# Kernel optimization log

Measured on AMD Instinct MI355X. Metric: run time of the kernel, lower is better.

The kernel has to match this reference:

```python
import jax, jax.numpy as jnp
import numpy as np

N = 50000      # nodes
E = 800000     # edges (avg degree 16)
IN = 128       # in_features
H = 4          # num_heads
OUT = 32       # out_features per head
NEG_SLOPE = 0.2


def setup_inputs() -> dict:
    key = jax.random.key(0)
    k1, k2, k3, k4 = jax.random.split(key, 4)
    h = jax.random.normal(k1, (N, IN), dtype=jnp.float32)
    edge_index = jax.random.randint(k2, (2, E), 0, N, dtype=jnp.int32)
    # xavier-ish init scales
    W = jax.random.normal(k3, (H, IN, OUT), dtype=jnp.float32) * np.float32(np.sqrt(2.0 / (IN + OUT)))
    a = jax.random.normal(k4, (H, 2 * OUT), dtype=jnp.float32) * np.float32(np.sqrt(2.0 / (2 * OUT)))
    return {"h": h, "edge_index": edge_index, "W": W, "a": a}


def reference(h, edge_index, W, a):
    src, dst = edge_index[0], edge_index[1]
    # project per head: [N, H, OUT]
    h_proj = jnp.einsum('ni,hio->nho', h, W)
    # score = leaky_relu(a . [Wh_src || Wh_dst]) ; split a to avoid materializing the concat
    a_src, a_dst = a[:, :OUT], a[:, OUT:]
    s_src = jnp.einsum('nho,ho->nh', h_proj, a_src)   # [N, H]
    s_dst = jnp.einsum('nho,ho->nh', h_proj, a_dst)   # [N, H]
    score = jax.nn.leaky_relu(s_src[src] + s_dst[dst], negative_slope=NEG_SLOPE)  # [E, H]
    # sparse softmax over incoming edges of each dst node
    smax = jax.ops.segment_max(score, dst, num_segments=N)          # [N, H]
    smax = jnp.where(jnp.isfinite(smax), smax, jnp.float32(-1e9))   # nodes with no in-edges
    score_exp = jnp.exp(score - smax[dst])                          # [E, H]
    denom = jax.ops.segment_sum(score_exp, dst, num_segments=N)     # [N, H]
    denom = jnp.maximum(denom, jnp.float32(1e-16))
    alpha = score_exp / denom[dst]                                  # [E, H]
    # weighted aggregation (dropout is identity in eval mode)
    h_src = h_proj[src]                                             # [E, H, OUT]
    h_out = jax.ops.segment_sum(alpha[:, :, None] * h_src, dst, num_segments=N)  # [N, H, OUT]
    h_out = h_out.reshape(N, H * OUT)  # concat=True
    return jax.nn.elu(h_out)
```

## Files before the change

kernel.cpp:

```cpp
#include <hip/hip_runtime.h>

#define NEG_SLOPE 0.2f
#define BCAP 8192

typedef __attribute__((ext_vector_type(8))) short short8;
typedef __attribute__((ext_vector_type(4))) float floatx4;

__device__ __forceinline__ unsigned f2bf(float x) {
  unsigned u = __float_as_uint(x);
  unsigned r = ((u >> 16) & 1u) + 0x7fffu;
  return (u + r) >> 16;
}
__device__ __forceinline__ float bf2f(unsigned hi16) {
  return __uint_as_float(hi16 << 16);
}

__global__ __launch_bounds__(256) void k_gemm(const float* __restrict__ h,
                                              const float* __restrict__ W,
                                              const float* __restrict__ a,
                                              const int* __restrict__ ei,
                                              int* __restrict__ bcur,
                                              unsigned* __restrict__ gpairs,
                                              unsigned short* __restrict__ hp16,
                                              float* __restrict__ ssrc,
                                              float* __restrict__ sdst,
                                              int N, int E, int NB1, int NB2) {
  __shared__ unsigned lds_u[16384];
  const int tid = threadIdx.x;

  if (blockIdx.x < NB1) {
    uint2* stage = (uint2*)lds_u;
    int* cnt = (int*)&lds_u[8192];
    int* start = (int*)&lds_u[8448];
    int* cur = (int*)&lds_u[8704];
    int* gbase = (int*)&lds_u[8960];
    int* scn = (int*)&lds_u[9216];
    const int e0 = blockIdx.x * 4096;
    for (int i = tid; i < NB2; i += 256) cnt[i] = 0;
    __syncthreads();
    int sarr[16], darr[16];
#pragma unroll
    for (int j = 0; j < 16; ++j) {
      int e = e0 + j * 256 + tid;
      if (e < E) {
        sarr[j] = ei[e];
        darr[j] = ei[E + e];
        atomicAdd(&cnt[darr[j] >> 8], 1);
      } else {
        darr[j] = -1;
      }
    }
    __syncthreads();
    int s = (tid < NB2) ? cnt[tid] : 0;
    scn[tid] = s;
    __syncthreads();
    for (int off = 1; off < 256; off <<= 1) {
      int t = (tid >= off) ? scn[tid - off] : 0;
      __syncthreads();
      scn[tid] += t;
      __syncthreads();
    }
    if (tid < NB2) {
      start[tid] = scn[tid] - s;
      cur[tid] = scn[tid] - s;
      gbase[tid] = s ? atomicAdd(&bcur[tid], s) : 0;
    }
    __syncthreads();
#pragma unroll
    for (int j = 0; j < 16; ++j) {
      if (darr[j] >= 0) {
        int b = darr[j] >> 8;
        int pos = atomicAdd(&cur[b], 1);
        stage[pos] = make_uint2((unsigned)sarr[j], (unsigned)darr[j]);
      }
    }
    __syncthreads();
    const int total = start[NB2 - 1] + cnt[NB2 - 1];
    for (int u = tid; u < total; u += 256) {
      uint2 pr = stage[u];
      int b = (int)(pr.y >> 8);
      gpairs[(size_t)b * BCAP + gbase[b] + (u - start[b])] =
          pr.x | ((pr.y & 255u) << 24);
    }
    __syncthreads();
  }

  const int lane = tid & 63;
  const int wv = tid >> 6;
  const int quad = lane >> 4;
  const int l16 = lane & 15;

#pragma unroll
  for (int it = 0; it < 8; ++it) {
    const int u = it * 256 + tid;
    const int ln = u & 63;
    const int kc = (u >> 6) & 3;
    const int ct = u >> 8;
    const int n = ct * 16 + (ln & 15);
    const int kb = kc * 32 + (ln >> 4) * 8;
    const int head = n >> 5;
    const float* src = W + head * 4096 + (size_t)kb * 32 + (n & 31);
    unsigned hi[4], lo[4];
#pragma unroll
    for (int jj = 0; jj < 4; ++jj) {
      float w0 = src[(2 * jj) * 32];
      float w1 = src[(2 * jj + 1) * 32];
      unsigned h0 = f2bf(w0), h1 = f2bf(w1);
      unsigned l0 = f2bf(w0 - bf2f(h0)), l1 = f2bf(w1 - bf2f(h1));
      hi[jj] = h0 | (h1 << 16);
      lo[jj] = l0 | (l1 << 16);
    }
    *(uint4*)&lds_u[u * 4] = make_uint4(hi[0], hi[1], hi[2], hi[3]);
    *(uint4*)&lds_u[8192 + u * 4] = make_uint4(lo[0], lo[1], lo[2], lo[3]);
  }

  const int row0 = blockIdx.x * 64;
  const int r = row0 + wv * 16 + l16;
  short8 Ah[4], Al[4];
#pragma unroll
  for (int kc = 0; kc < 4; ++kc) {
    float v[8];
    if (r < N) {
      float4 fa = *(const float4*)&h[(size_t)r * 128 + kc * 32 + quad * 8];
      float4 fb = *(const float4*)&h[(size_t)r * 128 + kc * 32 + quad * 8 + 4];
      v[0] = fa.x; v[1] = fa.y; v[2] = fa.z; v[3] = fa.w;
      v[4] = fb.x; v[5] = fb.y; v[6] = fb.z; v[7] = fb.w;
    } else {
#pragma unroll
      for (int j = 0; j < 8; ++j) v[j] = 0.f;
    }
#pragma unroll
    for (int j = 0; j < 8; ++j) {
      unsigned hi = f2bf(v[j]);
      Ah[kc][j] = (short)hi;
      Al[kc][j] = (short)f2bf(v[j] - bf2f(hi));
    }
  }
  __syncthreads();

  floatx4 C[8];
#pragma unroll
  for (int ct = 0; ct < 8; ++ct) {
    floatx4 c = {0.f, 0.f, 0.f, 0.f};
#pragma unroll
    for (int kc = 0; kc < 4; ++kc) {
      int bidx = ((ct * 4 + kc) * 64 + lane) * 4;
      short8 Bh, Bl;
      *(uint4*)&Bh = *(const uint4*)&lds_u[bidx];
      *(uint4*)&Bl = *(const uint4*)&lds_u[8192 + bidx];
      c = __builtin_amdgcn_mfma_f32_16x16x32_bf16(Ah[kc], Bh, c, 0, 0, 0);
      c = __builtin_amdgcn_mfma_f32_16x16x32_bf16(Al[kc], Bh, c, 0, 0, 0);
      c = __builtin_amdgcn_mfma_f32_16x16x32_bf16(Ah[kc], Bl, c, 0, 0, 0);
    }
    C[ct] = c;
  }
  __syncthreads();

  float* epi = (float*)lds_u;
#pragma unroll
  for (int ct = 0; ct < 8; ++ct) {
#pragma unroll
    for (int reg = 0; reg < 4; ++reg) {
      int rr = wv * 16 + quad * 4 + reg;
      epi[rr * 132 + ct * 16 + l16] = C[ct][reg];
    }
  }
  __syncthreads();

  const int row_l = tid >> 2;
  const int hh = tid & 3;
  const int rg = row0 + row_l;
  if (rg < N) {
    const float* rowp = &epi[row_l * 132 + hh * 32];
    float ss = 0.f, sd = 0.f;
    unsigned pka[16];
#pragma unroll
    for (int e = 0; e < 8; ++e) {
      float4 c4 = *(const float4*)&rowp[e * 4];
      float4 as = *(const float4*)&a[hh * 64 + e * 4];
      float4 ad = *(const float4*)&a[hh * 64 + 32 + e * 4];
      ss += c4.x * as.x + c4.y * as.y + c4.z * as.z + c4.w * as.w;
      sd += c4.x * ad.x + c4.y * ad.y + c4.z * ad.z + c4.w * ad.w;
      pka[e * 2] = f2bf(c4.x) | (f2bf(c4.y) << 16);
      pka[e * 2 + 1] = f2bf(c4.z) | (f2bf(c4.w) << 16);
    }
    unsigned short* dst = &hp16[(size_t)rg * 128 + hh * 32];
    *(uint4*)(dst) = make_uint4(pka[0], pka[1], pka[2], pka[3]);
    *(uint4*)(dst + 8) = make_uint4(pka[4], pka[5], pka[6], pka[7]);
    *(uint4*)(dst + 16) = make_uint4(pka[8], pka[9], pka[10], pka[11]);
    *(uint4*)(dst + 24) = make_uint4(pka[12], pka[13], pka[14], pka[15]);
    ssrc[(size_t)rg * 4 + hh] = ss;
    sdst[(size_t)rg * 4 + hh] = sd;
  }
}

__global__ __launch_bounds__(1024) void k_sortagg(const int* __restrict__ bcur,
                                                  const unsigned* __restrict__ gpairs,
                                                  const float* __restrict__ ssrc,
                                                  const float* __restrict__ sdst,
                                                  const uint4* __restrict__ hp4,
                                                  float* __restrict__ out, int N) {
  __shared__ int cnt2[128], start2[128], cur2[128], lds[128];
  __shared__ int srcsort[4096];
  __shared__ float sdl[512];
  const int tid = threadIdx.x;
  const int u0 = blockIdx.x;
  const int chunk = gridDim.x >> 3;
  const int id = ((gridDim.x & 7) == 0) ? (u0 & 7) * chunk + (u0 >> 3) : u0;
  const int b = id >> 1;
  const int half = id & 1;
  const size_t base = (size_t)b * BCAP;
  const int size = min(bcur[b], BCAP);
  const int d0s = (b << 8) + half * 128;
  const int ndst = min(128, N - d0s);

  if (tid < 128) cnt2[tid] = 0;
  for (int i = tid; i < ndst * 4; i += 1024) sdl[i] = sdst[(size_t)d0s * 4 + i];
  __syncthreads();

  unsigned pr[8];
  int rel[8];
#pragma unroll
  for (int j = 0; j < 8; ++j) {
    const int u = tid + j * 1024;
    pr[j] = (u < size) ? gpairs[base + u] : 0xffffffffu;
    rel[j] = (int)(pr[j] >> 24) - half * 128;
    if (pr[j] == 0xffffffffu || (unsigned)rel[j] >= 128u) rel[j] = -1;
  }
#pragma unroll
  for (int j = 0; j < 8; ++j)
    if (rel[j] >= 0) atomicAdd(&cnt2[rel[j]], 1);
  __syncthreads();

  if (tid < 128) lds[tid] = cnt2[tid];
  __syncthreads();
  for (int off = 1; off < 128; off <<= 1) {
    const int t = (tid < 128 && tid >= off) ? lds[tid - off] : 0;
    __syncthreads();
    if (tid < 128) lds[tid] += t;
    __syncthreads();
  }
  if (tid < 128) {
    start2[tid] = lds[tid] - cnt2[tid];
    cur2[tid] = lds[tid] - cnt2[tid];
  }
  __syncthreads();

#pragma unroll
  for (int j = 0; j < 8; ++j) {
    if (rel[j] >= 0) {
      const int pos = atomicAdd(&cur2[rel[j]], 1);
      srcsort[pos] = (int)(pr[j] & 0x00ffffffu);
    }
  }
  __syncthreads();

  const int l = tid & 15;
  const int hh = l >> 2;
  for (int dl = tid >> 4; dl < ndst; dl += 64) {
    const int d = d0s + dl;
    const int beg = start2[dl];
    const int end = beg + cnt2[dl];
    const float sdv = sdl[dl * 4 + hh];

    float den[4] = {0.f, 0.f, 0.f, 0.f};
    float acc[8];
#pragma unroll
    for (int j = 0; j < 8; ++j) acc[j] = 0.f;

    int p = beg;
    for (; p + 3 < end; p += 4) {
      int s[4];
      float w[4];
      uint4 v[4];
#pragma unroll
      for (int q = 0; q < 4; ++q) s[q] = srcsort[p + q];
#pragma unroll
      for (int q = 0; q < 4; ++q) {
        float x = ssrc[(size_t)s[q] * 4 + hh] + sdv;
        x = x >= 0.f ? x : NEG_SLOPE * x;
        w[q] = __expf(x);
        v[q] = hp4[(size_t)s[q] * 16 + l];
      }
#pragma unroll
      for (int q = 0; q < 4; ++q) {
        den[q] += w[q];
        acc[0] = fmaf(w[q], bf2f(v[q].x & 0xffffu), acc[0]);
        acc[1] = fmaf(w[q], bf2f(v[q].x >> 16), acc[1]);
        acc[2] = fmaf(w[q], bf2f(v[q].y & 0xffffu), acc[2]);
        acc[3] = fmaf(w[q], bf2f(v[q].y >> 16), acc[3]);
        acc[4] = fmaf(w[q], bf2f(v[q].z & 0xffffu), acc[4]);
        acc[5] = fmaf(w[q], bf2f(v[q].z >> 16), acc[5]);
        acc[6] = fmaf(w[q], bf2f(v[q].w & 0xffffu), acc[6]);
        acc[7] = fmaf(w[q], bf2f(v[q].w >> 16), acc[7]);
      }
    }
    for (; p < end; ++p) {
      const int s0 = srcsort[p];
      float x = ssrc[(size_t)s0 * 4 + hh] + sdv;
      x = x >= 0.f ? x : NEG_SLOPE * x;
      const float w0 = __expf(x);
      const uint4 v0 = hp4[(size_t)s0 * 16 + l];
      den[0] += w0;
      acc[0] = fmaf(w0, bf2f(v0.x & 0xffffu), acc[0]);
      acc[1] = fmaf(w0, bf2f(v0.x >> 16), acc[1]);
      acc[2] = fmaf(w0, bf2f(v0.y & 0xffffu), acc[2]);
      acc[3] = fmaf(w0, bf2f(v0.y >> 16), acc[3]);
      acc[4] = fmaf(w0, bf2f(v0.z & 0xffffu), acc[4]);
      acc[5] = fmaf(w0, bf2f(v0.z >> 16), acc[5]);
      acc[6] = fmaf(w0, bf2f(v0.w & 0xffffu), acc[6]);
      acc[7] = fmaf(w0, bf2f(v0.w >> 16), acc[7]);
    }
    const float rden = 1.f / fmaxf((den[0] + den[1]) + (den[2] + den[3]), 1e-16f);
    float o[8];
#pragma unroll
    for (int j = 0; j < 8; ++j) {
      const float x = acc[j] * rden;
      o[j] = x > 0.f ? x : expm1f(x);
    }
    float* dst = &out[(size_t)d * 128 + l * 8];
    *(float4*)dst = make_float4(o[0], o[1], o[2], o[3]);
    *(float4*)(dst + 4) = make_float4(o[4], o[5], o[6], o[7]);
  }
}

extern "C" void kernel_launch(void* const* d_in, const int* in_sizes, int n_in,
                              void* d_out, int out_size, void* d_ws, size_t ws_size,
                              hipStream_t stream) {
  const float* h = (const float*)d_in[0];
  const int* ei = (const int*)d_in[1];
  const float* W = (const float*)d_in[2];
  const float* a = (const float*)d_in[3];
  float* out = (float*)d_out;
  const int N = in_sizes[0] / 128;
  const int E = in_sizes[1] / 2;
  const int NB2 = (N + 255) >> 8;
  const int NB1 = (E + 4095) / 4096;
  const int NBG = max((N + 63) / 64, NB1);

  char* ws = (char*)d_ws;
  unsigned short* hp16 = (unsigned short*)ws;
  unsigned* gpairs = (unsigned*)(hp16 + (size_t)N * 128);
  float* ssrc = (float*)(gpairs + (size_t)NB2 * BCAP);
  float* sdst = ssrc + (size_t)N * 4;
  int* bcur = (int*)(sdst + (size_t)N * 4);

  hipMemsetAsync(bcur, 0, NB2 * sizeof(int), stream);
  k_gemm<<<NBG, 256, 0, stream>>>(h, W, a, ei, bcur, gpairs, hp16, ssrc, sdst,
                                  N, E, NB1, NB2);
  k_sortagg<<<NB2 * 2, 1024, 0, stream>>>(bcur, gpairs, ssrc, sdst,
                                          (const uint4*)hp16, out, N);
}
```

Before: 141.9 us.

## Split sort-aggregate into quarter-bucket blocks of 512 threads

Each destination bucket of 256 nodes is now handled by four 512-thread blocks of 64 destinations instead of two 1024-thread blocks of 128. The grid doubles, giving more, smaller blocks for better occupancy and load balance across CUs. The cost is that each block re-reads the whole bucket's pair list, so the gpairs reads grow from two passes per bucket to four blocks each scanning it twice. The register-held pairs become strided loops, and srcsort writes are clamped to SCAP for safety.

```diff
diff --git a/kernel.cpp b/kernel.cpp
--- a/kernel.cpp
+++ b/kernel.cpp
@@ -2,6 +2,7 @@
 
 #define NEG_SLOPE 0.2f
 #define BCAP 8192
+#define SCAP 4096
 
 typedef __attribute__((ext_vector_type(8))) short short8;
 typedef __attribute__((ext_vector_type(4))) float floatx4;
@@ -194,73 +195,69 @@
   }
 }
 
-__global__ __launch_bounds__(1024) void k_sortagg(const int* __restrict__ bcur,
-                                                  const unsigned* __restrict__ gpairs,
-                                                  const float* __restrict__ ssrc,
-                                                  const float* __restrict__ sdst,
-                                                  const uint4* __restrict__ hp4,
-                                                  float* __restrict__ out, int N) {
-  __shared__ int cnt2[128], start2[128], cur2[128], lds[128];
-  __shared__ int srcsort[4096];
-  __shared__ float sdl[512];
+__global__ __launch_bounds__(512) void k_sortagg(const int* __restrict__ bcur,
+                                                 const unsigned* __restrict__ gpairs,
+                                                 const float* __restrict__ ssrc,
+                                                 const float* __restrict__ sdst,
+                                                 const uint4* __restrict__ hp4,
+                                                 float* __restrict__ out, int N) {
+  __shared__ int cnt2[64], start2[64], cur2[64], lds[64];
+  __shared__ int srcsort[SCAP];
+  __shared__ float sdl[256];
   const int tid = threadIdx.x;
   const int u0 = blockIdx.x;
   const int chunk = gridDim.x >> 3;
   const int id = ((gridDim.x & 7) == 0) ? (u0 & 7) * chunk + (u0 >> 3) : u0;
-  const int b = id >> 1;
-  const int half = id & 1;
+  const int b = id >> 2;
+  const int quarter = id & 3;
   const size_t base = (size_t)b * BCAP;
   const int size = min(bcur[b], BCAP);
-  const int d0s = (b << 8) + half * 128;
-  const int ndst = min(128, N - d0s);
-
-  if (tid < 128) cnt2[tid] = 0;
-  for (int i = tid; i < ndst * 4; i += 1024) sdl[i] = sdst[(size_t)d0s * 4 + i];
-  __syncthreads();
-
-  unsigned pr[8];
-  int rel[8];
-#pragma unroll
-  for (int j = 0; j < 8; ++j) {
-    const int u = tid + j * 1024;
-    pr[j] = (u < size) ? gpairs[base + u] : 0xffffffffu;
-    rel[j] = (int)(pr[j] >> 24) - half * 128;
-    if (pr[j] == 0xffffffffu || (unsigned)rel[j] >= 128u) rel[j] = -1;
-  }
-#pragma unroll
-  for (int j = 0; j < 8; ++j)
-    if (rel[j] >= 0) atomicAdd(&cnt2[rel[j]], 1);
-  __syncthreads();
-
-  if (tid < 128) lds[tid] = cnt2[tid];
-  __syncthreads();
-  for (int off = 1; off < 128; off <<= 1) {
-    const int t = (tid < 128 && tid >= off) ? lds[tid - off] : 0;
-    __syncthreads();
-    if (tid < 128) lds[tid] += t;
-    __syncthreads();
-  }
-  if (tid < 128) {
+  const int q0 = quarter * 64;
+  const int d0s = (b << 8) + q0;
+  const int ndst = min(64, N - d0s);
+
+  if (tid < 64) cnt2[tid] = 0;
+  for (int i = tid; i < ndst * 4; i += 512) sdl[i] = sdst[(size_t)d0s * 4 + i];
+  __syncthreads();
+
+  for (int u = tid; u < size; u += 512) {
+    const int rel = (int)(gpairs[base + u] >> 24) - q0;
+    if ((unsigned)rel < 64u) atomicAdd(&cnt2[rel], 1);
+  }
+  __syncthreads();
+
+  if (tid < 64) lds[tid] = cnt2[tid];
+  __syncthreads();
+  for (int off = 1; off < 64; off <<= 1) {
+    const int t = (tid < 64 && tid >= off) ? lds[tid - off] : 0;
+    __syncthreads();
+    if (tid < 64) lds[tid] += t;
+    __syncthreads();
+  }
+  if (tid < 64) {
     start2[tid] = lds[tid] - cnt2[tid];
     cur2[tid] = lds[tid] - cnt2[tid];
   }
   __syncthreads();
 
-#pragma unroll
-  for (int j = 0; j < 8; ++j) {
-    if (rel[j] >= 0) {
-      const int pos = atomicAdd(&cur2[rel[j]], 1);
-      srcsort[pos] = (int)(pr[j] & 0x00ffffffu);
+  for (int u = tid; u < size; u += 512) {
+    const unsigned pr = gpairs[base + u];
+    const int rel = (int)(pr >> 24) - q0;
+    if ((unsigned)rel < 64u) {
+      const int pos = atomicAdd(&cur2[rel], 1);
+      if (pos < SCAP) srcsort[pos] = (int)(pr & 0x00ffffffu);
     }
   }
   __syncthreads();
 
   const int l = tid & 15;
   const int hh = l >> 2;
-  for (int dl = tid >> 4; dl < ndst; dl += 64) {
+  for (int dl = tid >> 4; dl < ndst; dl += 32) {
     const int d = d0s + dl;
-    const int beg = start2[dl];
-    const int end = beg + cnt2[dl];
+    int beg = start2[dl];
+    int end = beg + cnt2[dl];
+    beg = min(beg, SCAP);
+    end = min(end, SCAP);
     const float sdv = sdl[dl * 4 + hh];
 
     float den[4] = {0.f, 0.f, 0.f, 0.f};
@@ -348,6 +345,6 @@
   hipMemsetAsync(bcur, 0, NB2 * sizeof(int), stream);
   k_gemm<<<NBG, 256, 0, stream>>>(h, W, a, ei, bcur, gpairs, hp16, ssrc, sdst,
                                   N, E, NB1, NB2);
-  k_sortagg<<<NB2 * 2, 1024, 0, stream>>>(bcur, gpairs, ssrc, sdst,
-                                          (const uint4*)hp16, out, N);
-}
+  k_sortagg<<<NB2 * 4, 512, 0, stream>>>(bcur, gpairs, ssrc, sdst,
+                                         (const uint4*)hp16, out, N);
+}
```

New measurement: 144.0 us. No clear change (+1.4%).
